# Kernel optimization log

Hardware: AMD Instinct MI355X
Metric: run time of the kernel (lower is better)

## Reference

```python
import jax, jax.numpy as jnp
import numpy as np

N_WIRES = 8
N_QLAYERS = 1
DIM = 1 << N_WIRES  # 256

# bits[s, w] = w-th bit of basis state s; wire 0 is the MOST significant bit
# (torchquantum stores states as [bsz, 2, 2, ..., 2] with wire i at axis i+1)
_BITS = ((np.arange(DIM)[:, None] >> (N_WIRES - 1 - np.arange(N_WIRES))) & 1).astype(np.float32)


def setup_inputs() -> dict:
    key = jax.random.key(0)
    ks = jax.random.split(key, 5)
    pi = float(np.pi)
    return {
        "input_features": jax.random.normal(ks[0], (4, 4096, N_WIRES), jnp.float32),
        "params_ry1": jax.random.uniform(ks[1], (N_QLAYERS, N_WIRES), jnp.float32, -pi, pi),
        "params_crz1": jax.random.uniform(ks[2], (N_QLAYERS, N_WIRES), jnp.float32, -pi, pi),
        "params_ry2": jax.random.uniform(ks[3], (N_QLAYERS, N_WIRES), jnp.float32, -pi, pi),
        "params_crz2": jax.random.uniform(ks[4], (N_QLAYERS, N_WIRES), jnp.float32, -pi, pi),
    }


def _apply_ry(state, wire, theta):
    """Apply RY(theta) = [[c,-s],[s,c]] (c=cos(theta/2)) on `wire`.
    theta: scalar (shared param) or [B] (batched encoder angle)."""
    B = state.shape[0]
    c = jnp.cos(theta * 0.5)
    s = jnp.sin(theta * 0.5)
    if jnp.ndim(theta):  # per-batch angle
        c = c[:, None, None]
        s = s[:, None, None]
    st = state.reshape(B, 1 << wire, 2, -1)
    a, b = st[:, :, 0, :], st[:, :, 1, :]
    return jnp.stack([c * a - s * b, s * a + c * b], axis=2).reshape(B, DIM)


def _crz_block_diag(controls, targets, thetas, bits):
    """Fused diagonal of a commuting block of CRZ gates.
    CRZ(c,t,th) = diag over basis: 1 if bit_c==0 else exp(+/- i th/2) for bit_t=1/0.
    exponent contribution: bit_c * th * (bit_t - 0.5)."""
    expo = (bits[:, controls] * (bits[:, targets] - 0.5)) @ thetas  # [DIM]
    return jnp.exp(1j * expo).astype(jnp.complex64)


def _vqc_forward(x, params_ry1, params_crz1, params_ry2, params_crz2):
    B = x.shape[0]
    bits = jnp.asarray(_BITS)
    # |0...0>
    state = jnp.zeros((B, DIM), jnp.complex64).at[:, 0].set(1.0)

    idx = np.arange(N_WIRES)
    ctrl1, tgt1 = idx, (idx + 1) % N_WIRES  # crz block 1: wires [i, i+1]
    ctrl2, tgt2 = idx, (idx - 1) % N_WIRES  # crz block 2: wires [i, i-1]

    for k in range(N_QLAYERS):
        # tensor-product encoder: RY(x_i) on wire i
        for i in range(N_WIRES):
            state = _apply_ry(state, i, x[:, i])
        # CRZ ring (all diagonal -> fused)
        state = state * _crz_block_diag(ctrl1, tgt1, params_crz1[k], bits)[None, :]
        # trainable RY layer 1
        for i in range(N_WIRES):
            state = _apply_ry(state, i, params_ry1[k, i])
        # reverse CRZ ring (diagonal -> fused)
        state = state * _crz_block_diag(ctrl2, tgt2, params_crz2[k], bits)[None, :]
        # trainable RY layer 2
        for i in range(N_WIRES):
            state = _apply_ry(state, i, params_ry2[k, i])

    # PauliZ expectation on every wire: <Z_w> = sum_s |amp_s|^2 * (1 - 2*bit_w(s))
    probs = (state.real ** 2 + state.imag ** 2)  # [B, DIM]
    signs = 1.0 - 2.0 * bits                      # [DIM, N_WIRES]
    return probs @ signs                          # [B, N_WIRES]


def reference(input_features, params_ry1, params_crz1, params_ry2, params_crz2):
    bsz, slen, fz = input_features.shape
    x = input_features.reshape(-1, fz)
    out = _vqc_forward(x, params_ry1, params_crz1, params_ry2, params_crz2)
    return out.reshape(bsz, slen, fz)
```

## Files before the change

### kernel.cpp

```cpp
#include <hip/hip_runtime.h>
#include <math.h>

#define NW 8

typedef float v2f __attribute__((ext_vector_type(2)));

__device__ __forceinline__ v2f mk2(float a, float b) { v2f r; r.x = a; r.y = b; return r; }

template<int CTRL>
__device__ __forceinline__ float dpp_x(float v) {
    return __int_as_float(
        __builtin_amdgcn_update_dpp(0, __float_as_int(v), CTRL, 0xF, 0xF, true));
}
template<int CTRL>
__device__ __forceinline__ v2f dpp2(v2f v) {
    v2f r;
    r.x = dpp_x<CTRL>(v.x);
    r.y = dpp_x<CTRL>(v.y);
    return r;
}
#define XCH1(v) dpp2<0xB1>(v)
#define XCH2(v) dpp2<0x4E>(v)
#define XCH8(v) dpp2<0x128>(v)

__global__ __launch_bounds__(256, 2) void vqc_kernel(
    const float* __restrict__ x,
    const float* __restrict__ ry1,
    const float* __restrict__ crz1,
    const float* __restrict__ ry2,
    const float* __restrict__ crz2,
    float* __restrict__ out,
    int B)
{
    __shared__ __align__(16) float Tc1[288], Ts1[288], Tc2[288], Ts2[288];

    const int t = threadIdx.x;
    {
        const int n = t;
        float e1 = 0.f, e2 = 0.f;
#pragma unroll
        for (int i = 0; i < NW; ++i) {
            float bc  = (float)((n >> (7 - i)) & 1);
            float bt1 = (float)((n >> (7 - ((i + 1) & 7))) & 1);
            float bt2 = (float)((n >> (7 - ((i + 7) & 7))) & 1);
            e1 += bc * crz1[i] * (bt1 - 0.5f);
            e2 += bc * crz2[i] * (bt2 - 0.5f);
        }
        const int j = n & 31;
        const int u = (((n >> 7) & 1) << 2) | (((n >> 6) & 1) << 1) | ((n >> 5) & 1);
        const int idx = u * 36 + j;
        float s, c;
        __sincosf(e1, &s, &c);  Tc1[idx] = c;  Ts1[idx] = s;
        __sincosf(e2, &s, &c);  Tc2[idx] = c;  Ts2[idx] = s;
    }
    __syncthreads();

    const int lane = t & 63;
    const int u = ((lane & 1) << 2) | (((lane >> 1) & 1) << 1) | ((lane >> 3) & 1);
    const int g = ((lane >> 3) & 6) | ((lane >> 2) & 1);

    float rc1[8], rs1[8], rc2[8], rs2[8];
#pragma unroll
    for (int i = 0; i < 8; ++i) {
        __sincosf(0.5f * ry1[i], &rs1[i], &rc1[i]);
        __sincosf(0.5f * ry2[i], &rs2[i], &rc2[i]);
    }

    const float* pc1 = &Tc1[u * 36];
    const float* ps1 = &Ts1[u * 36];
    const float* pc2 = &Tc2[u * 36];
    const float* ps2 = &Ts2[u * 36];

    const int wavesPerBlock = blockDim.x >> 6;
    const int gwave = blockIdx.x * wavesPerBlock + (t >> 6);
    const int b  = gwave * 8 + g;
    const int bl = (b < B) ? b : (B - 1);

    const float4* xp = (const float4*)(x + (size_t)bl * NW);
    float4 xa = xp[0], xb = xp[1];
    float cs[8], sn[8];
    __sincosf(0.5f * xa.x, &sn[0], &cs[0]);
    __sincosf(0.5f * xa.y, &sn[1], &cs[1]);
    __sincosf(0.5f * xa.z, &sn[2], &cs[2]);
    __sincosf(0.5f * xa.w, &sn[3], &cs[3]);
    __sincosf(0.5f * xb.x, &sn[4], &cs[4]);
    __sincosf(0.5f * xb.y, &sn[5], &cs[5]);
    __sincosf(0.5f * xb.z, &sn[6], &cs[6]);
    __sincosf(0.5f * xb.w, &sn[7], &cs[7]);

    float pcf = ((lane & 1) ? sn[0] : cs[0])
              * ((lane & 2) ? sn[1] : cs[1])
              * ((lane & 8) ? sn[2] : cs[2]);

    float t2[2], t4[4], t8[8], t16[16];
    t2[0] = pcf * cs[3];  t2[1] = pcf * sn[3];
#pragma unroll
    for (int k = 0; k < 2; ++k)  { t4[2*k]  = t2[k] * cs[4];  t4[2*k+1]  = t2[k] * sn[4]; }
#pragma unroll
    for (int k = 0; k < 4; ++k)  { t8[2*k]  = t4[k] * cs[5];  t8[2*k+1]  = t4[k] * sn[5]; }
#pragma unroll
    for (int k = 0; k < 8; ++k)  { t16[2*k] = t8[k] * cs[6];  t16[2*k+1] = t8[k] * sn[6]; }

    const v2f cw7 = mk2(cs[7], sn[7]);
    v2f aP[16];
#pragma unroll
    for (int k = 0; k < 16; ++k) aP[k] = mk2(t16[k], t16[k]) * cw7;

    v2f reP[16], imP[16];
#pragma unroll
    for (int q = 0; q < 8; ++q) {
        float4 cq = *(const float4*)&pc1[4 * q];
        float4 sq = *(const float4*)&ps1[4 * q];
        v2f cl = mk2(cq.x, cq.y), ch = mk2(cq.z, cq.w);
        v2f sl = mk2(sq.x, sq.y), sh = mk2(sq.z, sq.w);
        reP[2*q]   = aP[2*q]   * cl;  imP[2*q]   = aP[2*q]   * sl;
        reP[2*q+1] = aP[2*q+1] * ch;  imP[2*q+1] = aP[2*q+1] * sh;
    }

#define CROSS_WIRE(RC, RS, WI, LBIT, EXCH)                                  \
    { float c_ = RC[WI], s_ = RS[WI];                                       \
      float se_ = (lane & LBIT) ? s_ : -s_;                                 \
      v2f cv = mk2(c_, c_), sev = mk2(se_, se_);                            \
      _Pragma("unroll")                                                     \
      for (int k = 0; k < 16; ++k) {                                        \
          v2f pre = EXCH(reP[k]);                                           \
          v2f pim = EXCH(imP[k]);                                           \
          reP[k] = reP[k] * cv + pre * sev;                                 \
          imP[k] = imP[k] * cv + pim * sev;                                 \
      } }

#define INLANE_WIRE(RC, RS, WI, M)                                          \
    { float c_ = RC[WI], s_ = RS[WI];                                       \
      v2f cv = mk2(c_, c_), sv = mk2(s_, s_);                               \
      _Pragma("unroll")                                                     \
      for (int k = 0; k < 16; ++k) if (!(k & M)) {                          \
          int h = k | M;                                                    \
          v2f rl = reP[k], rh = reP[h], il = imP[k], ih = imP[h];           \
          reP[k] = rl * cv - rh * sv;  reP[h] = rl * sv + rh * cv;          \
          imP[k] = il * cv - ih * sv;  imP[h] = il * sv + ih * cv;          \
      } }

#define WIRE7(RC, RS)                                                       \
    { float c_ = RC[7], s_ = RS[7];                                         \
      v2f cv = mk2(c_, c_), sev = mk2(-s_, s_);                             \
      _Pragma("unroll")                                                     \
      for (int k = 0; k < 16; ++k) {                                        \
          v2f r = reP[k], i = imP[k];                                       \
          v2f rsw = mk2(r.y, r.x), isw = mk2(i.y, i.x);                     \
          reP[k] = r * cv + rsw * sev;                                      \
          imP[k] = i * cv + isw * sev;                                      \
      } }

#define RY_LAYER(RC, RS)                                                    \
    do {                                                                    \
        CROSS_WIRE(RC, RS, 0, 1, XCH1);                                     \
        CROSS_WIRE(RC, RS, 1, 2, XCH2);                                     \
        CROSS_WIRE(RC, RS, 2, 8, XCH8);                                     \
        INLANE_WIRE(RC, RS, 3, 8);                                          \
        INLANE_WIRE(RC, RS, 4, 4);                                          \
        INLANE_WIRE(RC, RS, 5, 2);                                          \
        INLANE_WIRE(RC, RS, 6, 1);                                          \
        WIRE7(RC, RS);                                                      \
    } while (0)

    RY_LAYER(rc1, rs1);

#pragma unroll
    for (int q = 0; q < 8; ++q) {
        float4 cq = *(const float4*)&pc2[4 * q];
        float4 sq = *(const float4*)&ps2[4 * q];
        v2f cl = mk2(cq.x, cq.y), ch = mk2(cq.z, cq.w);
        v2f sl = mk2(sq.x, sq.y), sh = mk2(sq.z, sq.w);
        v2f r, i;
        r = reP[2*q];   i = imP[2*q];
        reP[2*q]   = r * cl - i * sl;  imP[2*q]   = r * sl + i * cl;
        r = reP[2*q+1]; i = imP[2*q+1];
        reP[2*q+1] = r * ch - i * sh;  imP[2*q+1] = r * sh + i * ch;
    }

    RY_LAYER(rc2, rs2);

    v2f pP[16];
#pragma unroll
    for (int k = 0; k < 16; ++k) pP[k] = reP[k] * reP[k] + imP[k] * imP[k];

    v2f s1v[8], dv6 = mk2(0.f, 0.f);
#pragma unroll
    for (int k = 0; k < 8; ++k) { s1v[k] = pP[2*k] + pP[2*k+1]; dv6 += pP[2*k] - pP[2*k+1]; }
    v2f s2v[4], dv5 = mk2(0.f, 0.f);
#pragma unroll
    for (int k = 0; k < 4; ++k) { s2v[k] = s1v[2*k] + s1v[2*k+1]; dv5 += s1v[2*k] - s1v[2*k+1]; }
    v2f s3v[2], dv4 = mk2(0.f, 0.f);
#pragma unroll
    for (int k = 0; k < 2; ++k) { s3v[k] = s2v[2*k] + s2v[2*k+1]; dv4 += s2v[2*k] - s2v[2*k+1]; }
    v2f sv0 = s3v[0] + s3v[1];
    v2f dv3 = s3v[0] - s3v[1];

    float v0 = sv0.x + sv0.y, d7 = sv0.x - sv0.y;
    float d3 = dv3.x + dv3.y, d4 = dv4.x + dv4.y;
    float d5 = dv5.x + dv5.y, d6 = dv6.x + dv6.y;

    v2f w1 = mk2(v0, d3), w2 = mk2(d4, d5), w3 = mk2(d6, d7);
#define BFLY_R(EXCH, M)                                                     \
    { v2f o1 = EXCH(w1), o2 = EXCH(w2), o3 = EXCH(w3);                      \
      if (lane & M) { w1 = o1 - w1; w2 = o2 - w2; w3 = o3 - w3; }           \
      else          { w1 = o1 + w1; w2 = o2 + w2; w3 = o3 + w3; } }
    BFLY_R(XCH1, 1);
    BFLY_R(XCH2, 2);
    BFLY_R(XCH8, 8);
#undef BFLY_R

    if (b < B) {
        const int loc = lane & 11;
        float* ob = out + (size_t)b * NW;
        if      (loc == 0) { ob[3] = w1.y; *(float4*)(ob + 4) = make_float4(w2.x, w2.y, w3.x, w3.y); }
        else if (loc == 1) ob[0] = w1.x;
        else if (loc == 2) ob[1] = w1.x;
        else if (loc == 8) ob[2] = w1.x;
    }
#undef RY_LAYER
#undef CROSS_WIRE
#undef INLANE_WIRE
#undef WIRE7
}

extern "C" void kernel_launch(void* const* d_in, const int* in_sizes, int n_in,
                              void* d_out, int out_size, void* d_ws, size_t ws_size,
                              hipStream_t stream) {
    const float* x    = (const float*)d_in[0];
    const float* ry1  = (const float*)d_in[1];
    const float* crz1 = (const float*)d_in[2];
    const float* ry2  = (const float*)d_in[3];
    const float* crz2 = (const float*)d_in[4];
    float* out = (float*)d_out;

    int B = in_sizes[0] / NW;
    int blocks = (B + 31) / 32;
    if (blocks < 1) blocks = 1;
    vqc_kernel<<<blocks, 256, 0, stream>>>(x, ry1, crz1, ry2, crz2, out, B);
}
```

Baseline: 68.97 us.

## Spread each statevector over 16 lanes instead of 8 to cut registers

The 256-amplitude state is now split across 16 lanes per batch element, 4 batch elements per wave, instead of 8 lanes per element and 8 per wave. Wire 3 becomes a cross-lane exchange built from two chained DPP ops, and the per-lane register state is halved. Launch bounds rise to 4 blocks per CU to exploit the lower register use, and the RY sincos values are computed once into shared memory. In exchange, the kernel runs twice as many blocks and does more cross-lane shuffles per sample.

New measurement: 69.63 us. About the same (+1.0%).

```diff
diff --git a/kernel.cpp b/kernel.cpp
--- a/kernel.cpp
+++ b/kernel.cpp
@@ -4,7 +4,6 @@
 #define NW 8
 
 typedef float v2f __attribute__((ext_vector_type(2)));
-
 __device__ __forceinline__ v2f mk2(float a, float b) { v2f r; r.x = a; r.y = b; return r; }
 
 template<int CTRL>
@@ -14,16 +13,14 @@
 }
 template<int CTRL>
 __device__ __forceinline__ v2f dpp2(v2f v) {
-    v2f r;
-    r.x = dpp_x<CTRL>(v.x);
-    r.y = dpp_x<CTRL>(v.y);
-    return r;
+    v2f r; r.x = dpp_x<CTRL>(v.x); r.y = dpp_x<CTRL>(v.y); return r;
 }
 #define XCH1(v) dpp2<0xB1>(v)
 #define XCH2(v) dpp2<0x4E>(v)
 #define XCH8(v) dpp2<0x128>(v)
-
-__global__ __launch_bounds__(256, 2) void vqc_kernel(
+#define XCH4(v) dpp2<0x1B>(dpp2<0x141>(v))
+
+__global__ __launch_bounds__(256, 4) void vqc_kernel(
     const float* __restrict__ x,
     const float* __restrict__ ry1,
     const float* __restrict__ crz1,
@@ -32,7 +29,8 @@
     float* __restrict__ out,
     int B)
 {
-    __shared__ __align__(16) float Tc1[288], Ts1[288], Tc2[288], Ts2[288];
+    __shared__ __align__(16) float Tc1[320], Ts1[320], Tc2[320], Ts2[320];
+    __shared__ __align__(16) float Rp[32];
 
     const int t = threadIdx.x;
     {
@@ -46,34 +44,36 @@
             e1 += bc * crz1[i] * (bt1 - 0.5f);
             e2 += bc * crz2[i] * (bt2 - 0.5f);
         }
-        const int j = n & 31;
-        const int u = (((n >> 7) & 1) << 2) | (((n >> 6) & 1) << 1) | ((n >> 5) & 1);
-        const int idx = u * 36 + j;
+        const int j  = n & 15;
+        const int sl = ((n >> 7) & 1) | (((n >> 6) & 1) << 1)
+                     | (((n >> 4) & 1) << 2) | (((n >> 5) & 1) << 3);
+        const int idx = sl * 20 + j;
         float s, c;
         __sincosf(e1, &s, &c);  Tc1[idx] = c;  Ts1[idx] = s;
         __sincosf(e2, &s, &c);  Tc2[idx] = c;  Ts2[idx] = s;
+        if (t < 8)       { __sincosf(0.5f * ry1[t], &s, &c);     Rp[t] = c;      Rp[8 + t] = s; }
+        else if (t < 16) { __sincosf(0.5f * ry2[t - 8], &s, &c); Rp[8 + t] = c;  Rp[16 + t] = s; }
     }
     __syncthreads();
 
     const int lane = t & 63;
-    const int u = ((lane & 1) << 2) | (((lane >> 1) & 1) << 1) | ((lane >> 3) & 1);
-    const int g = ((lane >> 3) & 6) | ((lane >> 2) & 1);
+    const int sl   = lane & 15;
+    const int g    = lane >> 4;
 
     float rc1[8], rs1[8], rc2[8], rs2[8];
-#pragma unroll
-    for (int i = 0; i < 8; ++i) {
-        __sincosf(0.5f * ry1[i], &rs1[i], &rc1[i]);
-        __sincosf(0.5f * ry2[i], &rs2[i], &rc2[i]);
-    }
-
-    const float* pc1 = &Tc1[u * 36];
-    const float* ps1 = &Ts1[u * 36];
-    const float* pc2 = &Tc2[u * 36];
-    const float* ps2 = &Ts2[u * 36];
+    *(float4*)&rc1[0] = *(const float4*)&Rp[0];  *(float4*)&rc1[4] = *(const float4*)&Rp[4];
+    *(float4*)&rs1[0] = *(const float4*)&Rp[8];  *(float4*)&rs1[4] = *(const float4*)&Rp[12];
+    *(float4*)&rc2[0] = *(const float4*)&Rp[16]; *(float4*)&rc2[4] = *(const float4*)&Rp[20];
+    *(float4*)&rs2[0] = *(const float4*)&Rp[24]; *(float4*)&rs2[4] = *(const float4*)&Rp[28];
+
+    const float* pc1 = &Tc1[sl * 20];
+    const float* ps1 = &Ts1[sl * 20];
+    const float* pc2 = &Tc2[sl * 20];
+    const float* ps2 = &Ts2[sl * 20];
 
     const int wavesPerBlock = blockDim.x >> 6;
     const int gwave = blockIdx.x * wavesPerBlock + (t >> 6);
-    const int b  = gwave * 8 + g;
+    const int b  = gwave * 4 + g;
     const int bl = (b < B) ? b : (B - 1);
 
     const float4* xp = (const float4*)(x + (size_t)bl * NW);
@@ -88,41 +88,40 @@
     __sincosf(0.5f * xb.z, &sn[6], &cs[6]);
     __sincosf(0.5f * xb.w, &sn[7], &cs[7]);
 
-    float pcf = ((lane & 1) ? sn[0] : cs[0])
-              * ((lane & 2) ? sn[1] : cs[1])
-              * ((lane & 8) ? sn[2] : cs[2]);
-
-    float t2[2], t4[4], t8[8], t16[16];
-    t2[0] = pcf * cs[3];  t2[1] = pcf * sn[3];
-#pragma unroll
-    for (int k = 0; k < 2; ++k)  { t4[2*k]  = t2[k] * cs[4];  t4[2*k+1]  = t2[k] * sn[4]; }
-#pragma unroll
-    for (int k = 0; k < 4; ++k)  { t8[2*k]  = t4[k] * cs[5];  t8[2*k+1]  = t4[k] * sn[5]; }
-#pragma unroll
-    for (int k = 0; k < 8; ++k)  { t16[2*k] = t8[k] * cs[6];  t16[2*k+1] = t8[k] * sn[6]; }
+    float pcf = ((sl & 1) ? sn[0] : cs[0])
+              * ((sl & 2) ? sn[1] : cs[1])
+              * ((sl & 8) ? sn[2] : cs[2])
+              * ((sl & 4) ? sn[3] : cs[3]);
+
+    float t2[2], t4[4], t8[8];
+    t2[0] = pcf * cs[4];  t2[1] = pcf * sn[4];
+#pragma unroll
+    for (int k = 0; k < 2; ++k) { t4[2*k] = t2[k] * cs[5];  t4[2*k+1] = t2[k] * sn[5]; }
+#pragma unroll
+    for (int k = 0; k < 4; ++k) { t8[2*k] = t4[k] * cs[6];  t8[2*k+1] = t4[k] * sn[6]; }
 
     const v2f cw7 = mk2(cs[7], sn[7]);
-    v2f aP[16];
-#pragma unroll
-    for (int k = 0; k < 16; ++k) aP[k] = mk2(t16[k], t16[k]) * cw7;
-
-    v2f reP[16], imP[16];
-#pragma unroll
-    for (int q = 0; q < 8; ++q) {
+    v2f aP[8];
+#pragma unroll
+    for (int k = 0; k < 8; ++k) aP[k] = mk2(t8[k], t8[k]) * cw7;
+
+    v2f reP[8], imP[8];
+#pragma unroll
+    for (int q = 0; q < 4; ++q) {
         float4 cq = *(const float4*)&pc1[4 * q];
         float4 sq = *(const float4*)&ps1[4 * q];
         v2f cl = mk2(cq.x, cq.y), ch = mk2(cq.z, cq.w);
-        v2f sl = mk2(sq.x, sq.y), sh = mk2(sq.z, sq.w);
-        reP[2*q]   = aP[2*q]   * cl;  imP[2*q]   = aP[2*q]   * sl;
+        v2f sl_ = mk2(sq.x, sq.y), sh = mk2(sq.z, sq.w);
+        reP[2*q]   = aP[2*q]   * cl;  imP[2*q]   = aP[2*q]   * sl_;
         reP[2*q+1] = aP[2*q+1] * ch;  imP[2*q+1] = aP[2*q+1] * sh;
     }
 
 #define CROSS_WIRE(RC, RS, WI, LBIT, EXCH)                                  \
     { float c_ = RC[WI], s_ = RS[WI];                                       \
-      float se_ = (lane & LBIT) ? s_ : -s_;                                 \
+      float se_ = (sl & LBIT) ? s_ : -s_;                                   \
       v2f cv = mk2(c_, c_), sev = mk2(se_, se_);                            \
       _Pragma("unroll")                                                     \
-      for (int k = 0; k < 16; ++k) {                                        \
+      for (int k = 0; k < 8; ++k) {                                         \
           v2f pre = EXCH(reP[k]);                                           \
           v2f pim = EXCH(imP[k]);                                           \
           reP[k] = reP[k] * cv + pre * sev;                                 \
@@ -133,7 +132,7 @@
     { float c_ = RC[WI], s_ = RS[WI];                                       \
       v2f cv = mk2(c_, c_), sv = mk2(s_, s_);                               \
       _Pragma("unroll")                                                     \
-      for (int k = 0; k < 16; ++k) if (!(k & M)) {                          \
+      for (int k = 0; k < 8; ++k) if (!(k & M)) {                           \
           int h = k | M;                                                    \
           v2f rl = reP[k], rh = reP[h], il = imP[k], ih = imP[h];           \
           reP[k] = rl * cv - rh * sv;  reP[h] = rl * sv + rh * cv;          \
@@ -144,7 +143,7 @@
     { float c_ = RC[7], s_ = RS[7];                                         \
       v2f cv = mk2(c_, c_), sev = mk2(-s_, s_);                             \
       _Pragma("unroll")                                                     \
-      for (int k = 0; k < 16; ++k) {                                        \
+      for (int k = 0; k < 8; ++k) {                                         \
           v2f r = reP[k], i = imP[k];                                       \
           v2f rsw = mk2(r.y, r.x), isw = mk2(i.y, i.x);                     \
           reP[k] = r * cv + rsw * sev;                                      \
@@ -156,7 +155,7 @@
         CROSS_WIRE(RC, RS, 0, 1, XCH1);                                     \
         CROSS_WIRE(RC, RS, 1, 2, XCH2);                                     \
         CROSS_WIRE(RC, RS, 2, 8, XCH8);                                     \
-        INLANE_WIRE(RC, RS, 3, 8);                                          \
+        CROSS_WIRE(RC, RS, 3, 4, XCH4);                                     \
         INLANE_WIRE(RC, RS, 4, 4);                                          \
         INLANE_WIRE(RC, RS, 5, 2);                                          \
         INLANE_WIRE(RC, RS, 6, 1);                                          \
@@ -166,57 +165,59 @@
     RY_LAYER(rc1, rs1);
 
 #pragma unroll
-    for (int q = 0; q < 8; ++q) {
+    for (int q = 0; q < 4; ++q) {
         float4 cq = *(const float4*)&pc2[4 * q];
         float4 sq = *(const float4*)&ps2[4 * q];
         v2f cl = mk2(cq.x, cq.y), ch = mk2(cq.z, cq.w);
-        v2f sl = mk2(sq.x, sq.y), sh = mk2(sq.z, sq.w);
+        v2f sl_ = mk2(sq.x, sq.y), sh = mk2(sq.z, sq.w);
         v2f r, i;
         r = reP[2*q];   i = imP[2*q];
-        reP[2*q]   = r * cl - i * sl;  imP[2*q]   = r * sl + i * cl;
+        reP[2*q]   = r * cl - i * sl_;  imP[2*q]   = r * sl_ + i * cl;
         r = reP[2*q+1]; i = imP[2*q+1];
-        reP[2*q+1] = r * ch - i * sh;  imP[2*q+1] = r * sh + i * ch;
+        reP[2*q+1] = r * ch - i * sh;   imP[2*q+1] = r * sh + i * ch;
     }
 
     RY_LAYER(rc2, rs2);
 
-    v2f pP[16];
-#pragma unroll
-    for (int k = 0; k < 16; ++k) pP[k] = reP[k] * reP[k] + imP[k] * imP[k];
-
-    v2f s1v[8], dv6 = mk2(0.f, 0.f);
-#pragma unroll
-    for (int k = 0; k < 8; ++k) { s1v[k] = pP[2*k] + pP[2*k+1]; dv6 += pP[2*k] - pP[2*k+1]; }
-    v2f s2v[4], dv5 = mk2(0.f, 0.f);
-#pragma unroll
-    for (int k = 0; k < 4; ++k) { s2v[k] = s1v[2*k] + s1v[2*k+1]; dv5 += s1v[2*k] - s1v[2*k+1]; }
-    v2f s3v[2], dv4 = mk2(0.f, 0.f);
-#pragma unroll
-    for (int k = 0; k < 2; ++k) { s3v[k] = s2v[2*k] + s2v[2*k+1]; dv4 += s2v[2*k] - s2v[2*k+1]; }
-    v2f sv0 = s3v[0] + s3v[1];
-    v2f dv3 = s3v[0] - s3v[1];
+    v2f pP[8];
+#pragma unroll
+    for (int k = 0; k < 8; ++k) pP[k] = reP[k] * reP[k] + imP[k] * imP[k];
+
+    v2f s1v[4], dv6 = mk2(0.f, 0.f);
+#pragma unroll
+    for (int m = 0; m < 4; ++m) { s1v[m] = pP[2*m] + pP[2*m+1]; dv6 += pP[2*m] - pP[2*m+1]; }
+    v2f s2v[2], dv5 = mk2(0.f, 0.f);
+#pragma unroll
+    for (int m = 0; m < 2; ++m) { s2v[m] = s1v[2*m] + s1v[2*m+1]; dv5 += s1v[2*m] - s1v[2*m+1]; }
+    v2f sv0 = s2v[0] + s2v[1];
+    v2f dv4 = s2v[0] - s2v[1];
 
     float v0 = sv0.x + sv0.y, d7 = sv0.x - sv0.y;
-    float d3 = dv3.x + dv3.y, d4 = dv4.x + dv4.y;
-    float d5 = dv5.x + dv5.y, d6 = dv6.x + dv6.y;
-
-    v2f w1 = mk2(v0, d3), w2 = mk2(d4, d5), w3 = mk2(d6, d7);
-#define BFLY_R(EXCH, M)                                                     \
-    { v2f o1 = EXCH(w1), o2 = EXCH(w2), o3 = EXCH(w3);                      \
-      if (lane & M) { w1 = o1 - w1; w2 = o2 - w2; w3 = o3 - w3; }           \
-      else          { w1 = o1 + w1; w2 = o2 + w2; w3 = o3 + w3; } }
-    BFLY_R(XCH1, 1);
-    BFLY_R(XCH2, 2);
-    BFLY_R(XCH8, 8);
+    float d4 = dv4.x + dv4.y, d5 = dv5.x + dv5.y, d6 = dv6.x + dv6.y;
+
+    v2f w1 = mk2(v0, d4), w2 = mk2(d5, d6);
+    float w3 = d7;
+#define BFLY_R(EXCH, EXCHS, M)                                              \
+    { v2f o1 = EXCH(w1), o2 = EXCH(w2); float o3 = EXCHS(w3);               \
+      if (sl & M) { w1 = o1 - w1; w2 = o2 - w2; w3 = o3 - w3; }             \
+      else        { w1 = o1 + w1; w2 = o2 + w2; w3 = o3 + w3; } }
+#define XS1(v) dpp_x<0xB1>(v)
+#define XS2(v) dpp_x<0x4E>(v)
+#define XS8(v) dpp_x<0x128>(v)
+#define XS4(v) dpp_x<0x1B>(dpp_x<0x141>(v))
+    BFLY_R(XCH1, XS1, 1);
+    BFLY_R(XCH2, XS2, 2);
+    BFLY_R(XCH4, XS4, 4);
+    BFLY_R(XCH8, XS8, 8);
 #undef BFLY_R
 
     if (b < B) {
-        const int loc = lane & 11;
         float* ob = out + (size_t)b * NW;
-        if      (loc == 0) { ob[3] = w1.y; *(float4*)(ob + 4) = make_float4(w2.x, w2.y, w3.x, w3.y); }
-        else if (loc == 1) ob[0] = w1.x;
-        else if (loc == 2) ob[1] = w1.x;
-        else if (loc == 8) ob[2] = w1.x;
+        if      (sl == 0) *(float4*)(ob + 4) = make_float4(w1.y, w2.x, w2.y, w3);
+        else if (sl == 1) ob[0] = w1.x;
+        else if (sl == 2) ob[1] = w1.x;
+        else if (sl == 8) ob[2] = w1.x;
+        else if (sl == 4) ob[3] = w1.x;
     }
 #undef RY_LAYER
 #undef CROSS_WIRE
@@ -235,7 +236,7 @@
     float* out = (float*)d_out;
 
     int B = in_sizes[0] / NW;
-    int blocks = (B + 31) / 32;
+    int blocks = (B + 15) / 16;
     if (blocks < 1) blocks = 1;
     vqc_kernel<<<blocks, 256, 0, stream>>>(x, ry1, crz1, ry2, crz2, out, B);
 }
```
